# Performance work log

Measured on AMD Instinct MI355X. Metric: run time of the kernel, lower is better.

## Reference

```python
import jax, jax.numpy as jnp
import numpy as np

V = 500000
VD = 256
G = 4000
H = 8
GD = 256
HIDDEN = 128


def setup_inputs() -> dict:
    key = jax.random.key(0)
    ks = jax.random.split(key, 6)
    node_embeddings = jax.random.normal(ks[0], (V, VD), dtype=jnp.float32)
    node_to_graph_map = jnp.sort(jax.random.randint(ks[1], (V,), 0, G, dtype=jnp.int32))
    scale = lambda fan_in: 1.0 / np.sqrt(fan_in)
    scoring_w1 = jax.random.normal(ks[2], (VD, HIDDEN), dtype=jnp.float32) * scale(VD)
    scoring_w2 = jax.random.normal(ks[3], (HIDDEN, H), dtype=jnp.float32) * scale(HIDDEN)
    transform_w1 = jax.random.normal(ks[4], (VD, HIDDEN), dtype=jnp.float32) * scale(VD)
    transform_w2 = jax.random.normal(ks[5], (HIDDEN, GD), dtype=jnp.float32) * scale(HIDDEN)
    return {
        "node_embeddings": node_embeddings,
        "node_to_graph_map": node_to_graph_map,
        "num_graphs": G,
        "scoring_w1": scoring_w1,
        "scoring_w2": scoring_w2,
        "transform_w1": transform_w1,
        "transform_w2": transform_w2,
    }


def _segment_softmax(logits, segment_ids, num_segments):
    # logits: [V, H]; softmax over nodes within each graph, per head.
    seg_max = jax.ops.segment_max(logits, segment_ids, num_segments=num_segments)
    seg_max = jnp.where(jnp.isfinite(seg_max), seg_max, 0.0)
    exp = jnp.exp(logits - seg_max[segment_ids])
    denom = jax.ops.segment_sum(exp, segment_ids, num_segments=num_segments)
    return exp / denom[segment_ids]


def reference(node_embeddings, node_to_graph_map, num_graphs,
              scoring_w1, scoring_w2, transform_w1, transform_w2):
    # Scoring MLP (hidden ReLU, linear out, no biases): [V, H]
    scores = jax.nn.relu(node_embeddings @ scoring_w1) @ scoring_w2
    # Per-graph softmax weights, per head: [V, H]
    weights = _segment_softmax(scores, node_to_graph_map, num_graphs)
    # Transformation MLP, then the call() applies the activation to the MLP output.
    node_reprs = jax.nn.relu(jax.nn.relu(node_embeddings @ transform_w1) @ transform_w2)  # [V, GD]
    node_reprs = node_reprs.reshape(-1, H, GD // H)  # [V, H, GD/H]
    weighted = (weights[:, :, None] * node_reprs).reshape(-1, GD)  # [V, GD]
    graph_reprs = jax.ops.segment_sum(weighted, node_to_graph_map, num_segments=num_graphs)
    return graph_reprs
```

## Files before the change

### kernel.cpp

```cpp
#include <hip/hip_runtime.h>
#include <hip/hip_fp16.h>

#define VD 256
#define HID 128
#define GD 256
#define NH 8
#define NGRAPH 4000
#define RT 64

typedef _Float16 f16;
typedef f16 f16x4 __attribute__((ext_vector_type(4)));
typedef f16 f16x8 __attribute__((ext_vector_type(8)));
typedef float f32x4 __attribute__((ext_vector_type(4)));

__device__ __forceinline__ f16x8 load_a_frag(const float* p) {
  float4 p0 = *(const float4*)(p);
  float4 p1 = *(const float4*)(p + 4);
  f16x8 v;
  v[0] = (f16)p0.x; v[1] = (f16)p0.y; v[2] = (f16)p0.z; v[3] = (f16)p0.w;
  v[4] = (f16)p1.x; v[5] = (f16)p1.y; v[6] = (f16)p1.z; v[7] = (f16)p1.w;
  return v;
}

__device__ __forceinline__ void pack_b_dev(const float* __restrict__ src,
                                           f16* __restrict__ dst,
                                           int K, int Nsrc, int Ndst, int t) {
  int NB = Ndst / 16, KB = K / 32;
  int total = KB * NB * 64;
  if (t >= total) return;
  int lane = t & 63;
  int frag = t >> 6;
  int nb = frag % NB, kb = frag / NB;
  int col = nb * 16 + (lane & 15);
  int krow = kb * 32 + (lane >> 4) * 8;
  f16x8 o;
  #pragma unroll
  for (int i = 0; i < 8; ++i) {
    float v = (col < Nsrc) ? src[(size_t)(krow + i) * Nsrc + col] : 0.0f;
    o[i] = (f16)v;
  }
  *(f16x8*)(dst + (size_t)t * 8) = o;
}

__global__ __launch_bounds__(256) void k_prep(
    const float* __restrict__ w1s, const float* __restrict__ w1t,
    const float* __restrict__ w2t, const float* __restrict__ w2s,
    const int* __restrict__ map,
    f16* __restrict__ W1sp, f16* __restrict__ W1tp,
    f16* __restrict__ W2tp, f16* __restrict__ W2sp,
    int* __restrict__ gs, int V, int G) {
  int b = blockIdx.x;
  int tid = threadIdx.x;
  if (b < 16) {
    pack_b_dev(w1s, W1sp, VD, HID, HID, b * 256 + tid);
  } else if (b < 32) {
    pack_b_dev(w1t, W1tp, VD, HID, HID, (b - 16) * 256 + tid);
  } else if (b < 48) {
    pack_b_dev(w2t, W2tp, HID, GD, GD, (b - 32) * 256 + tid);
  } else if (b == 48) {
    pack_b_dev(w2s, W2sp, HID, NH, 16, tid);
  } else {
    int g = (b - 49) * 256 + tid;
    if (g > G) return;
    int lo = 0, hi = V;
    while (lo < hi) {
      int mid = (lo + hi) >> 1;
      if (map[mid] < g) lo = mid + 1; else hi = mid;
    }
    gs[g] = lo;
  }
}

__global__ __attribute__((amdgpu_flat_work_group_size(512, 512),
                          amdgpu_waves_per_eu(4, 4))) void k_stage1(
    const float* __restrict__ E, int V, int ntiles,
    const f16* __restrict__ W1sp, const f16* __restrict__ W2sp,
    const f16* __restrict__ W1tp,
    float* __restrict__ scores, f16* __restrict__ ht) {
  __shared__ __attribute__((aligned(16))) f16 lE[RT][VD + 8];
  __shared__ __attribute__((aligned(16))) f16 lH[RT][HID + 8];
  __shared__ __attribute__((aligned(16))) f16 lT[RT][HID + 8];
  const int tid = threadIdx.x;
  const int wave = tid >> 6;
  const int lane = tid & 63;
  const int hi = lane >> 4;
  const int lo = lane & 15;
  const int srow = tid >> 6;
  const int scol = (tid & 63) * 4;

  f16x8 Bs[8], Bt[8];
  #pragma unroll
  for (int kb = 0; kb < 8; ++kb) {
    Bs[kb] = *(const f16x8*)(W1sp + ((size_t)(kb * 8 + wave) * 64 + lane) * 8);
    Bt[kb] = *(const f16x8*)(W1tp + ((size_t)(kb * 8 + wave) * 64 + lane) * 8);
  }

  int t = blockIdx.x;
  if (t >= ntiles) return;
  const int stride = gridDim.x;

  float4 pf[8];
  {
    const int r0 = t * RT;
    #pragma unroll
    for (int p = 0; p < 8; ++p) {
      int grow = r0 + p * 8 + srow;
      pf[p] = (grow < V) ? *(const float4*)(E + (size_t)grow * VD + scol)
                         : make_float4(0.f, 0.f, 0.f, 0.f);
    }
  }

  while (t < ntiles) {
    const int r0 = t * RT;
    #pragma unroll
    for (int p = 0; p < 8; ++p) {
      f16x4 h;
      h[0] = (f16)pf[p].x; h[1] = (f16)pf[p].y;
      h[2] = (f16)pf[p].z; h[3] = (f16)pf[p].w;
      *(f16x4*)&lE[p * 8 + srow][scol] = h;
    }
    const int tn = t + stride;
    if (tn < ntiles) {
      const int rn = tn * RT;
      #pragma unroll
      for (int p = 0; p < 8; ++p) {
        int grow = rn + p * 8 + srow;
        pf[p] = (grow < V) ? *(const float4*)(E + (size_t)grow * VD + scol)
                           : make_float4(0.f, 0.f, 0.f, 0.f);
      }
    }
    __syncthreads();

    #pragma unroll
    for (int m = 0; m < 4; ++m) {
      f32x4 as = {0.f, 0.f, 0.f, 0.f};
      f32x4 at = {0.f, 0.f, 0.f, 0.f};
      #pragma unroll
      for (int kb = 0; kb < 8; ++kb) {
        f16x8 a = *(const f16x8*)&lE[m * 16 + lo][kb * 32 + hi * 8];
        as = __builtin_amdgcn_mfma_f32_16x16x32_f16(a, Bs[kb], as, 0, 0, 0);
        at = __builtin_amdgcn_mfma_f32_16x16x32_f16(a, Bt[kb], at, 0, 0, 0);
      }
      #pragma unroll
      for (int r = 0; r < 4; ++r) {
        lH[m * 16 + hi * 4 + r][wave * 16 + lo] = (f16)fmaxf(as[r], 0.f);
        if (ht != nullptr)
          lT[m * 16 + hi * 4 + r][wave * 16 + lo] = (f16)fmaxf(at[r], 0.f);
      }
    }
    __syncthreads();

    if (wave < 4) {
      f16x8 a2[4];
      #pragma unroll
      for (int kb = 0; kb < 4; ++kb)
        a2[kb] = *(const f16x8*)&lH[wave * 16 + lo][kb * 32 + hi * 8];
      f32x4 acc = {0.f, 0.f, 0.f, 0.f};
      #pragma unroll
      for (int kb = 0; kb < 4; ++kb) {
        f16x8 b = *(const f16x8*)(W2sp + ((size_t)kb * 64 + lane) * 8);
        acc = __builtin_amdgcn_mfma_f32_16x16x32_f16(a2[kb], b, acc, 0, 0, 0);
      }
      if (lo < NH) {
        #pragma unroll
        for (int r = 0; r < 4; ++r) {
          int row = r0 + wave * 16 + hi * 4 + r;
          if (row < V) scores[(size_t)row * NH + lo] = acc[r];
        }
      }
    }

    if (ht != nullptr) {
      #pragma unroll
      for (int p = 0; p < 2; ++p) {
        int c = p * 512 + tid;
        int row = c >> 4;
        int col = (c & 15) * 8;
        int grow = r0 + row;
        if (grow < V)
          *(f16x8*)(ht + (size_t)grow * HID + col) = *(const f16x8*)&lT[row][col];
      }
    }
    t = tn;
  }
}

__global__ __launch_bounds__(256, 4) void k_graph(
    const f16* __restrict__ ht, const float* __restrict__ scores,
    const f16* __restrict__ W2tp, const int* __restrict__ gs,
    float* __restrict__ out, int V) {
  __shared__ float red[4][NH];
  const int g = blockIdx.x;
  const int tid = threadIdx.x;
  const int wave = tid >> 6;
  const int lane = tid & 63;
  const int hi = lane >> 4;
  const int lo = lane & 15;
  const int s = gs[g], e = gs[g + 1];

  f16x8 b[4][4];
  #pragma unroll
  for (int j = 0; j < 4; ++j)
    #pragma unroll
    for (int kb = 0; kb < 4; ++kb)
      b[j][kb] = *(const f16x8*)(
          W2tp + ((size_t)(kb * 16 + wave * 4 + j) * 64 + lane) * 8);

  float mx[NH];
  #pragma unroll
  for (int h = 0; h < NH; ++h) mx[h] = -1e30f;
  for (int i = s + tid; i < e; i += 256) {
    float4 s0 = *(const float4*)(scores + (size_t)i * NH);
    float4 s1 = *(const float4*)(scores + (size_t)i * NH + 4);
    mx[0] = fmaxf(mx[0], s0.x); mx[1] = fmaxf(mx[1], s0.y);
    mx[2] = fmaxf(mx[2], s0.z); mx[3] = fmaxf(mx[3], s0.w);
    mx[4] = fmaxf(mx[4], s1.x); mx[5] = fmaxf(mx[5], s1.y);
    mx[6] = fmaxf(mx[6], s1.z); mx[7] = fmaxf(mx[7], s1.w);
  }
  #pragma unroll
  for (int off = 32; off >= 1; off >>= 1)
    #pragma unroll
    for (int h = 0; h < NH; ++h) mx[h] = fmaxf(mx[h], __shfl_xor(mx[h], off));
  if (lane == 0) {
    #pragma unroll
    for (int h = 0; h < NH; ++h) red[wave][h] = mx[h];
  }
  __syncthreads();
  #pragma unroll
  for (int h = 0; h < NH; ++h)
    mx[h] = fmaxf(fmaxf(red[0][h], red[1][h]), fmaxf(red[2][h], red[3][h]));
  __syncthreads();

  float sm[NH];
  #pragma unroll
  for (int h = 0; h < NH; ++h) sm[h] = 0.f;
  for (int i = s + tid; i < e; i += 256) {
    float4 s0 = *(const float4*)(scores + (size_t)i * NH);
    float4 s1 = *(const float4*)(scores + (size_t)i * NH + 4);
    sm[0] += __expf(s0.x - mx[0]); sm[1] += __expf(s0.y - mx[1]);
    sm[2] += __expf(s0.z - mx[2]); sm[3] += __expf(s0.w - mx[3]);
    sm[4] += __expf(s1.x - mx[4]); sm[5] += __expf(s1.y - mx[5]);
    sm[6] += __expf(s1.z - mx[6]); sm[7] += __expf(s1.w - mx[7]);
  }
  #pragma unroll
  for (int off = 32; off >= 1; off >>= 1)
    #pragma unroll
    for (int h = 0; h < NH; ++h) sm[h] += __shfl_xor(sm[h], off);
  if (lane == 0) {
    #pragma unroll
    for (int h = 0; h < NH; ++h) red[wave][h] = sm[h];
  }
  __syncthreads();

  const int h0 = wave * 2, h1 = wave * 2 + 1;
  const float m0 = mx[h0], m1 = mx[h1];
  const float ri0 = 1.f / (red[0][h0] + red[1][h0] + red[2][h0] + red[3][h0]);
  const float ri1 = 1.f / (red[0][h1] + red[1][h1] + red[2][h1] + red[3][h1]);

  float vsum[4] = {0.f, 0.f, 0.f, 0.f};

  for (int cb = s; cb < e; cb += 16) {
    f16x8 a[4];
    int arow = cb + lo;
    int ar = arow < V ? arow : V - 1;
    #pragma unroll
    for (int kb = 0; kb < 4; ++kb)
      a[kb] = *(const f16x8*)(ht + (size_t)ar * HID + kb * 32 + hi * 8);

    int wr = cb + hi * 4;
    float wv[2][4];
    #pragma unroll
    for (int r = 0; r < 4; ++r) {
      int row = wr + r;
      bool in = row < e;
      float sc0 = in ? scores[(size_t)row * NH + h0] : 0.f;
      float sc1 = in ? scores[(size_t)row * NH + h1] : 0.f;
      wv[0][r] = in ? __expf(sc0 - m0) * ri0 : 0.f;
      wv[1][r] = in ? __expf(sc1 - m1) * ri1 : 0.f;
    }
    #pragma unroll
    for (int j = 0; j < 4; ++j) {
      f32x4 acc = {0.f, 0.f, 0.f, 0.f};
      #pragma unroll
      for (int kb = 0; kb < 4; ++kb)
        acc = __builtin_amdgcn_mfma_f32_16x16x32_f16(a[kb], b[j][kb], acc, 0, 0, 0);
      const float* wvp = wv[j >> 1];
      float v = 0.f;
      #pragma unroll
      for (int r = 0; r < 4; ++r) v += fmaxf(acc[r], 0.f) * wvp[r];
      vsum[j] += v;
    }
  }

  #pragma unroll
  for (int j = 0; j < 4; ++j) {
    float v = vsum[j];
    v += __shfl_xor(v, 16);
    v += __shfl_xor(v, 32);
    if (lane < 16) out[(size_t)g * GD + (wave * 4 + j) * 16 + lo] = v;
  }
}

__global__ __launch_bounds__(64) void k_stats(
    float* __restrict__ scores, const int* __restrict__ gs) {
  int g = blockIdx.x;
  int lane = threadIdx.x;
  int s = gs[g], e = gs[g + 1];
  if (e <= s) return;
  float mx[NH];
  #pragma unroll
  for (int h = 0; h < NH; ++h) mx[h] = -1e30f;
  for (int i = s + lane; i < e; i += 64) {
    float4 s0 = *(const float4*)(scores + (size_t)i * NH);
    float4 s1 = *(const float4*)(scores + (size_t)i * NH + 4);
    mx[0] = fmaxf(mx[0], s0.x); mx[1] = fmaxf(mx[1], s0.y);
    mx[2] = fmaxf(mx[2], s0.z); mx[3] = fmaxf(mx[3], s0.w);
    mx[4] = fmaxf(mx[4], s1.x); mx[5] = fmaxf(mx[5], s1.y);
    mx[6] = fmaxf(mx[6], s1.z); mx[7] = fmaxf(mx[7], s1.w);
  }
  #pragma unroll
  for (int off = 32; off >= 1; off >>= 1)
    #pragma unroll
    for (int h = 0; h < NH; ++h) mx[h] = fmaxf(mx[h], __shfl_xor(mx[h], off));
  float sm[NH];
  #pragma unroll
  for (int h = 0; h < NH; ++h) sm[h] = 0.f;
  for (int i = s + lane; i < e; i += 64) {
    float4 s0 = *(const float4*)(scores + (size_t)i * NH);
    float4 s1 = *(const float4*)(scores + (size_t)i * NH + 4);
    sm[0] += __expf(s0.x - mx[0]); sm[1] += __expf(s0.y - mx[1]);
    sm[2] += __expf(s0.z - mx[2]); sm[3] += __expf(s0.w - mx[3]);
    sm[4] += __expf(s1.x - mx[4]); sm[5] += __expf(s1.y - mx[5]);
    sm[6] += __expf(s1.z - mx[6]); sm[7] += __expf(s1.w - mx[7]);
  }
  #pragma unroll
  for (int off = 32; off >= 1; off >>= 1)
    #pragma unroll
    for (int h = 0; h < NH; ++h) sm[h] += __shfl_xor(sm[h], off);
  float rinv[NH];
  #pragma unroll
  for (int h = 0; h < NH; ++h) rinv[h] = 1.f / sm[h];
  for (int i = s + lane; i < e; i += 64) {
    float4 s0 = *(const float4*)(scores + (size_t)i * NH);
    float4 s1 = *(const float4*)(scores + (size_t)i * NH + 4);
    s0.x = __expf(s0.x - mx[0]) * rinv[0]; s0.y = __expf(s0.y - mx[1]) * rinv[1];
    s0.z = __expf(s0.z - mx[2]) * rinv[2]; s0.w = __expf(s0.w - mx[3]) * rinv[3];
    s1.x = __expf(s1.x - mx[4]) * rinv[4]; s1.y = __expf(s1.y - mx[5]) * rinv[5];
    s1.z = __expf(s1.z - mx[6]) * rinv[6]; s1.w = __expf(s1.w - mx[7]) * rinv[7];
    *(float4*)(scores + (size_t)i * NH) = s0;
    *(float4*)(scores + (size_t)i * NH + 4) = s1;
  }
}

__global__ __launch_bounds__(256, 2) void k_transform2(
    const float* __restrict__ E, int V,
    const f16* __restrict__ W1tp, const f16* __restrict__ W2tp,
    const float* __restrict__ w, const int* __restrict__ gs,
    float* __restrict__ out) {
  __shared__ f16 hl[16][HID + 8];
  const int g = blockIdx.x;
  const int wave = threadIdx.x >> 6;
  const int lane = threadIdx.x & 63;
  const int hi = lane >> 4;
  const int lo = lane & 15;
  const int s = gs[g], e = gs[g + 1];

  f16x8 b[4][4];
  #pragma unroll
  for (int j = 0; j < 4; ++j)
    #pragma unroll
    for (int kb = 0; kb < 4; ++kb)
      b[j][kb] = *(const f16x8*)(
          W2tp + ((size_t)(kb * 16 + wave * 4 + j) * 64 + lane) * 8);

  float vsum[4] = {0.f, 0.f, 0.f, 0.f};

  for (int cb = s; cb < e; cb += 16) {
    int arow = cb + lo;
    int ar = arow < V ? arow : V - 1;
    f16x8 a[8];
    const float* ep = E + (size_t)ar * VD + hi * 8;
    #pragma unroll
    for (int kb = 0; kb < 8; ++kb) a[kb] = load_a_frag(ep + kb * 32);

    __syncthreads();
    #pragma unroll
    for (int nn = 0; nn < 2; ++nn) {
      int n = wave * 2 + nn;
      f32x4 acc = {0.f, 0.f, 0.f, 0.f};
      #pragma unroll
      for (int kb = 0; kb < 8; ++kb) {
        f16x8 bb = *(const f16x8*)(W1tp + ((size_t)(kb * 8 + n) * 64 + lane) * 8);
        acc = __builtin_amdgcn_mfma_f32_16x16x32_f16(a[kb], bb, acc, 0, 0, 0);
      }
      #pragma unroll
      for (int r = 0; r < 4; ++r)
        hl[hi * 4 + r][n * 16 + lo] = (f16)fmaxf(acc[r], 0.f);
    }
    __syncthreads();

    int wr = cb + hi * 4;
    float wv[2][4];
    #pragma unroll
    for (int hh = 0; hh < 2; ++hh) {
      int head = wave * 2 + hh;
      #pragma unroll
      for (int r = 0; r < 4; ++r) {
        int row = wr + r;
        wv[hh][r] = (row < e) ? w[(size_t)row * NH + head] : 0.f;
      }
    }
    f16x8 a2[4];
    #pragma unroll
    for (int kb = 0; kb < 4; ++kb)
      a2[kb] = *(const f16x8*)&hl[lo][kb * 32 + hi * 8];
    #pragma unroll
    for (int j = 0; j < 4; ++j) {
      f32x4 acc = {0.f, 0.f, 0.f, 0.f};
      #pragma unroll
      for (int kb = 0; kb < 4; ++kb)
        acc = __builtin_amdgcn_mfma_f32_16x16x32_f16(a2[kb], b[j][kb], acc, 0, 0, 0);
      const float* wvp = wv[j >> 1];
      float v = 0.f;
      #pragma unroll
      for (int r = 0; r < 4; ++r) v += fmaxf(acc[r], 0.f) * wvp[r];
      vsum[j] += v;
    }
  }

  #pragma unroll
  for (int j = 0; j < 4; ++j) {
    float v = vsum[j];
    v += __shfl_xor(v, 16);
    v += __shfl_xor(v, 32);
    if (lane < 16) out[(size_t)g * GD + (wave * 4 + j) * 16 + lo] = v;
  }
}

extern "C" void kernel_launch(void* const* d_in, const int* in_sizes, int n_in,
                              void* d_out, int out_size, void* d_ws, size_t ws_size,
                              hipStream_t stream) {
  const float* E   = (const float*)d_in[0];
  const int*   map = (const int*)d_in[1];
  const float* w1s = (const float*)d_in[3];
  const float* w2s = (const float*)d_in[4];
  const float* w1t = (const float*)d_in[5];
  const float* w2t = (const float*)d_in[6];
  const int V = in_sizes[0] / VD;
  const int G = NGRAPH;

  char* ws = (char*)d_ws;
  size_t off = 0;
  float* scores = (float*)(ws + off); off += (size_t)V * NH * 4;
  int* gs = (int*)(ws + off); off += (size_t)(G + 1) * 4;
  off = (off + 255) & ~(size_t)255;
  f16* W1sp = (f16*)(ws + off); off += (size_t)VD * HID * 2;
  f16* W1tp = (f16*)(ws + off); off += (size_t)VD * HID * 2;
  f16* W2tp = (f16*)(ws + off); off += (size_t)HID * GD * 2;
  f16* W2sp = (f16*)(ws + off); off += (size_t)HID * 16 * 2;
  off = (off + 255) & ~(size_t)255;
  f16* ht = (f16*)(ws + off);
  const size_t need_fused = off + (size_t)V * HID * 2;
  const bool fused = ws_size >= need_fused;

  k_prep<<<65, 256, 0, stream>>>(w1s, w1t, w2t, w2s, map,
                                 W1sp, W1tp, W2tp, W2sp, gs, V, G);

  const int ntiles = (V + RT - 1) / RT;
  const int grid1 = (ntiles + 3) / 4;
  k_stage1<<<grid1, 512, 0, stream>>>(
      E, V, ntiles, W1sp, W2sp, W1tp, scores, fused ? ht : nullptr);

  if (fused) {
    k_graph<<<G, 256, 0, stream>>>(ht, scores, W2tp, gs, (float*)d_out, V);
  } else {
    k_stats<<<G, 64, 0, stream>>>(scores, gs);
    k_transform2<<<G, 256, 0, stream>>>(E, V, W1tp, W2tp, scores, gs,
                                        (float*)d_out);
  }
}
```

Baseline: 288.5 us.

## Stage per-graph softmax weights in LDS and reorder score store after ht write

```diff
diff --git a/kernel.cpp b/kernel.cpp
--- a/kernel.cpp
+++ b/kernel.cpp
@@ -7,6 +7,7 @@
 #define NH 8
 #define NGRAPH 4000
 #define RT 64
+#define MAXROWS 512
 
 typedef _Float16 f16;
 typedef f16 f16x4 __attribute__((ext_vector_type(4)));
@@ -150,26 +151,6 @@
     }
     __syncthreads();
 
-    if (wave < 4) {
-      f16x8 a2[4];
-      #pragma unroll
-      for (int kb = 0; kb < 4; ++kb)
-        a2[kb] = *(const f16x8*)&lH[wave * 16 + lo][kb * 32 + hi * 8];
-      f32x4 acc = {0.f, 0.f, 0.f, 0.f};
-      #pragma unroll
-      for (int kb = 0; kb < 4; ++kb) {
-        f16x8 b = *(const f16x8*)(W2sp + ((size_t)kb * 64 + lane) * 8);
-        acc = __builtin_amdgcn_mfma_f32_16x16x32_f16(a2[kb], b, acc, 0, 0, 0);
-      }
-      if (lo < NH) {
-        #pragma unroll
-        for (int r = 0; r < 4; ++r) {
-          int row = r0 + wave * 16 + hi * 4 + r;
-          if (row < V) scores[(size_t)row * NH + lo] = acc[r];
-        }
-      }
-    }
-
     if (ht != nullptr) {
       #pragma unroll
       for (int p = 0; p < 2; ++p) {
@@ -181,15 +162,37 @@
           *(f16x8*)(ht + (size_t)grow * HID + col) = *(const f16x8*)&lT[row][col];
       }
     }
+
+    if (wave < 4) {
+      f16x8 a2[4];
+      #pragma unroll
+      for (int kb = 0; kb < 4; ++kb)
+        a2[kb] = *(const f16x8*)&lH[wave * 16 + lo][kb * 32 + hi * 8];
+      f32x4 acc = {0.f, 0.f, 0.f, 0.f};
+      #pragma unroll
+      for (int kb = 0; kb < 4; ++kb) {
+        f16x8 b = *(const f16x8*)(W2sp + ((size_t)kb * 64 + lane) * 8);
+        acc = __builtin_amdgcn_mfma_f32_16x16x32_f16(a2[kb], b, acc, 0, 0, 0);
+      }
+      if (lo < NH) {
+        #pragma unroll
+        for (int r = 0; r < 4; ++r) {
+          int row = r0 + wave * 16 + hi * 4 + r;
+          if (row < V) scores[(size_t)row * NH + lo] = acc[r];
+        }
+      }
+    }
     t = tn;
   }
 }
 
-__global__ __launch_bounds__(256, 4) void k_graph(
+__global__ __attribute__((amdgpu_flat_work_group_size(256, 256),
+                          amdgpu_waves_per_eu(4, 4))) void k_graph(
     const f16* __restrict__ ht, const float* __restrict__ scores,
     const f16* __restrict__ W2tp, const int* __restrict__ gs,
     float* __restrict__ out, int V) {
   __shared__ float red[4][NH];
+  __shared__ float lW[MAXROWS * NH];
   const int g = blockIdx.x;
   const int tid = threadIdx.x;
   const int wave = tid >> 6;
@@ -197,6 +200,12 @@
   const int hi = lane >> 4;
   const int lo = lane & 15;
   const int s = gs[g], e = gs[g + 1];
+  const int n = e - s;
+
+  if (n <= 0) {
+    out[(size_t)g * GD + tid] = 0.f;
+    return;
+  }
 
   f16x8 b[4][4];
   #pragma unroll
@@ -206,56 +215,115 @@
       b[j][kb] = *(const f16x8*)(
           W2tp + ((size_t)(kb * 16 + wave * 4 + j) * 64 + lane) * 8);
 
-  float mx[NH];
-  #pragma unroll
-  for (int h = 0; h < NH; ++h) mx[h] = -1e30f;
-  for (int i = s + tid; i < e; i += 256) {
-    float4 s0 = *(const float4*)(scores + (size_t)i * NH);
-    float4 s1 = *(const float4*)(scores + (size_t)i * NH + 4);
-    mx[0] = fmaxf(mx[0], s0.x); mx[1] = fmaxf(mx[1], s0.y);
-    mx[2] = fmaxf(mx[2], s0.z); mx[3] = fmaxf(mx[3], s0.w);
-    mx[4] = fmaxf(mx[4], s1.x); mx[5] = fmaxf(mx[5], s1.y);
-    mx[6] = fmaxf(mx[6], s1.z); mx[7] = fmaxf(mx[7], s1.w);
-  }
-  #pragma unroll
-  for (int off = 32; off >= 1; off >>= 1)
-    #pragma unroll
-    for (int h = 0; h < NH; ++h) mx[h] = fmaxf(mx[h], __shfl_xor(mx[h], off));
-  if (lane == 0) {
-    #pragma unroll
-    for (int h = 0; h < NH; ++h) red[wave][h] = mx[h];
-  }
-  __syncthreads();
-  #pragma unroll
-  for (int h = 0; h < NH; ++h)
-    mx[h] = fmaxf(fmaxf(red[0][h], red[1][h]), fmaxf(red[2][h], red[3][h]));
-  __syncthreads();
-
-  float sm[NH];
-  #pragma unroll
-  for (int h = 0; h < NH; ++h) sm[h] = 0.f;
-  for (int i = s + tid; i < e; i += 256) {
-    float4 s0 = *(const float4*)(scores + (size_t)i * NH);
-    float4 s1 = *(const float4*)(scores + (size_t)i * NH + 4);
-    sm[0] += __expf(s0.x - mx[0]); sm[1] += __expf(s0.y - mx[1]);
-    sm[2] += __expf(s0.z - mx[2]); sm[3] += __expf(s0.w - mx[3]);
-    sm[4] += __expf(s1.x - mx[4]); sm[5] += __expf(s1.y - mx[5]);
-    sm[6] += __expf(s1.z - mx[6]); sm[7] += __expf(s1.w - mx[7]);
-  }
-  #pragma unroll
-  for (int off = 32; off >= 1; off >>= 1)
-    #pragma unroll
-    for (int h = 0; h < NH; ++h) sm[h] += __shfl_xor(sm[h], off);
-  if (lane == 0) {
-    #pragma unroll
-    for (int h = 0; h < NH; ++h) red[wave][h] = sm[h];
-  }
-  __syncthreads();
-
   const int h0 = wave * 2, h1 = wave * 2 + 1;
-  const float m0 = mx[h0], m1 = mx[h1];
-  const float ri0 = 1.f / (red[0][h0] + red[1][h0] + red[2][h0] + red[3][h0]);
-  const float ri1 = 1.f / (red[0][h1] + red[1][h1] + red[2][h1] + red[3][h1]);
+  float m0, m1, ri0, ri1;
+  const bool use_lds = (n <= MAXROWS);
+
+  if (use_lds) {
+    for (int c = tid; c < n * 2; c += 256)
+      *(float4*)&lW[c * 4] = *(const float4*)(scores + (size_t)s * NH + c * 4);
+    __syncthreads();
+
+    float mx[NH];
+    #pragma unroll
+    for (int h = 0; h < NH; ++h) mx[h] = -1e30f;
+    for (int i = tid; i < n; i += 256) {
+      #pragma unroll
+      for (int h = 0; h < NH; ++h) mx[h] = fmaxf(mx[h], lW[i * NH + h]);
+    }
+    #pragma unroll
+    for (int off = 32; off >= 1; off >>= 1)
+      #pragma unroll
+      for (int h = 0; h < NH; ++h) mx[h] = fmaxf(mx[h], __shfl_xor(mx[h], off));
+    if (lane == 0) {
+      #pragma unroll
+      for (int h = 0; h < NH; ++h) red[wave][h] = mx[h];
+    }
+    __syncthreads();
+    #pragma unroll
+    for (int h = 0; h < NH; ++h)
+      mx[h] = fmaxf(fmaxf(red[0][h], red[1][h]), fmaxf(red[2][h], red[3][h]));
+    __syncthreads();
+
+    float sm[NH];
+    #pragma unroll
+    for (int h = 0; h < NH; ++h) sm[h] = 0.f;
+    for (int i = tid; i < n; i += 256) {
+      #pragma unroll
+      for (int h = 0; h < NH; ++h) sm[h] += __expf(lW[i * NH + h] - mx[h]);
+    }
+    #pragma unroll
+    for (int off = 32; off >= 1; off >>= 1)
+      #pragma unroll
+      for (int h = 0; h < NH; ++h) sm[h] += __shfl_xor(sm[h], off);
+    if (lane == 0) {
+      #pragma unroll
+      for (int h = 0; h < NH; ++h) red[wave][h] = sm[h];
+    }
+    __syncthreads();
+
+    float rinv[NH];
+    #pragma unroll
+    for (int h = 0; h < NH; ++h)
+      rinv[h] = 1.f / (red[0][h] + red[1][h] + red[2][h] + red[3][h]);
+
+    for (int i = tid; i < n; i += 256) {
+      #pragma unroll
+      for (int h = 0; h < NH; ++h)
+        lW[i * NH + h] = __expf(lW[i * NH + h] - mx[h]) * rinv[h];
+    }
+    __syncthreads();
+    m0 = mx[h0]; m1 = mx[h1]; ri0 = rinv[h0]; ri1 = rinv[h1];
+  } else {
+    float mx[NH];
+    #pragma unroll
+    for (int h = 0; h < NH; ++h) mx[h] = -1e30f;
+    for (int i = s + tid; i < e; i += 256) {
+      float4 s0 = *(const float4*)(scores + (size_t)i * NH);
+      float4 s1 = *(const float4*)(scores + (size_t)i * NH + 4);
+      mx[0] = fmaxf(mx[0], s0.x); mx[1] = fmaxf(mx[1], s0.y);
+      mx[2] = fmaxf(mx[2], s0.z); mx[3] = fmaxf(mx[3], s0.w);
+      mx[4] = fmaxf(mx[4], s1.x); mx[5] = fmaxf(mx[5], s1.y);
+      mx[6] = fmaxf(mx[6], s1.z); mx[7] = fmaxf(mx[7], s1.w);
+    }
+    #pragma unroll
+    for (int off = 32; off >= 1; off >>= 1)
+      #pragma unroll
+      for (int h = 0; h < NH; ++h) mx[h] = fmaxf(mx[h], __shfl_xor(mx[h], off));
+    if (lane == 0) {
+      #pragma unroll
+      for (int h = 0; h < NH; ++h) red[wave][h] = mx[h];
+    }
+    __syncthreads();
+    #pragma unroll
+    for (int h = 0; h < NH; ++h)
+      mx[h] = fmaxf(fmaxf(red[0][h], red[1][h]), fmaxf(red[2][h], red[3][h]));
+    __syncthreads();
+
+    float sm[NH];
+    #pragma unroll
+    for (int h = 0; h < NH; ++h) sm[h] = 0.f;
+    for (int i = s + tid; i < e; i += 256) {
+      float4 s0 = *(const float4*)(scores + (size_t)i * NH);
+      float4 s1 = *(const float4*)(scores + (size_t)i * NH + 4);
+      sm[0] += __expf(s0.x - mx[0]); sm[1] += __expf(s0.y - mx[1]);
+      sm[2] += __expf(s0.z - mx[2]); sm[3] += __expf(s0.w - mx[3]);
+      sm[4] += __expf(s1.x - mx[4]); sm[5] += __expf(s1.y - mx[5]);
+      sm[6] += __expf(s1.z - mx[6]); sm[7] += __expf(s1.w - mx[7]);
+    }
+    #pragma unroll
+    for (int off = 32; off >= 1; off >>= 1)
+      #pragma unroll
+      for (int h = 0; h < NH; ++h) sm[h] += __shfl_xor(sm[h], off);
+    if (lane == 0) {
+      #pragma unroll
+      for (int h = 0; h < NH; ++h) red[wave][h] = sm[h];
+    }
+    __syncthreads();
+    m0 = mx[h0]; m1 = mx[h1];
+    ri0 = 1.f / (red[0][h0] + red[1][h0] + red[2][h0] + red[3][h0]);
+    ri1 = 1.f / (red[0][h1] + red[1][h1] + red[2][h1] + red[3][h1]);
+  }
 
   float vsum[4] = {0.f, 0.f, 0.f, 0.f};
 
@@ -269,14 +337,25 @@
 
     int wr = cb + hi * 4;
     float wv[2][4];
-    #pragma unroll
-    for (int r = 0; r < 4; ++r) {
-      int row = wr + r;
-      bool in = row < e;
-      float sc0 = in ? scores[(size_t)row * NH + h0] : 0.f;
-      float sc1 = in ? scores[(size_t)row * NH + h1] : 0.f;
-      wv[0][r] = in ? __expf(sc0 - m0) * ri0 : 0.f;
-      wv[1][r] = in ? __expf(sc1 - m1) * ri1 : 0.f;
+    if (use_lds) {
+      #pragma unroll
+      for (int r = 0; r < 4; ++r) {
+        int row = wr + r;
+        bool in = row < e;
+        int rel = in ? (row - s) : 0;
+        wv[0][r] = in ? lW[rel * NH + h0] : 0.f;
+        wv[1][r] = in ? lW[rel * NH + h1] : 0.f;
+      }
+    } else {
+      #pragma unroll
+      for (int r = 0; r < 4; ++r) {
+        int row = wr + r;
+        bool in = row < e;
+        float sc0 = in ? scores[(size_t)row * NH + h0] : 0.f;
+        float sc1 = in ? scores[(size_t)row * NH + h1] : 0.f;
+        wv[0][r] = in ? __expf(sc0 - m0) * ri0 : 0.f;
+        wv[1][r] = in ? __expf(sc1 - m1) * ri1 : 0.f;
+      }
     }
     #pragma unroll
     for (int j = 0; j < 4; ++j) {
```

Result: faster. 263.5 us (-8.6%).
